# Optimization experiments

Hardware: AMD Instinct MI355X
Metric: run time of the kernel (lower is better)

Reference implementation:

```python
import jax, jax.numpy as jnp
import numpy as np

NEG_BIG = -9e15
ALPHA = 0.2  # LeakyReLU negative slope
B, N, F_IN, F_OUT = 8, 2048, 128, 128


def setup_inputs() -> dict:
    key = jax.random.key(0)
    k1, k2, k3, k4 = jax.random.split(key, 4)
    inp = jax.random.normal(k1, (B, N, F_IN), dtype=jnp.float32)
    adj = jax.random.randint(k2, (B, N, N), 0, 2, dtype=jnp.int32)
    W = 0.02 * jax.random.normal(k3, (F_OUT, F_IN), dtype=jnp.float32)  # nn.Linear weight [out,in]
    a = 0.02 * jax.random.normal(k4, (1, 2 * F_OUT), dtype=jnp.float32)  # attention vector [1, 2F]
    return {"input": inp, "adj": adj, "W": W, "a": a}


def reference(input, adj, W, a):
    # h = input @ W^T : [B, N, F_OUT]
    h = jnp.einsum("bnf,of->bno", input, W)
    f_out = h.shape[-1]
    # Decompose a . [h_i || h_j] = (h_i . a1) + (h_j . a2) -- same math as the
    # explicit repeat_interleave/repeat/cat, without the O(N^2 * 2F) tensor.
    a1 = a[0, :f_out]
    a2 = a[0, f_out:]
    s1 = h @ a1  # [B, N] score for source node i
    s2 = h @ a2  # [B, N] score for target node j
    e = jax.nn.leaky_relu(s1[:, :, None] + s2[:, None, :], negative_slope=ALPHA)  # [B,N,N]
    masked = jnp.where(adj > 0, e, NEG_BIG)
    attention = jax.nn.softmax(masked, axis=-1)
    # dropout p=0.0 (eval) -> identity
    h_prime = jnp.einsum("bnm,bmo->bno", attention, h)
    return h_prime
```

## Files before the change

kernel.cpp:

```cpp
#include <hip/hip_runtime.h>
#include <stdint.h>


#define B_ 8
#define N_ 2048
#define FD 128
#define ALPHA_ 0.2f
#define TJ 64
#define NCHUNK (N_ / TJ)
#define CHUNK_U4 1024

typedef __attribute__((ext_vector_type(8))) short short8;
typedef __attribute__((ext_vector_type(4))) float f32x4;

#define HCHUNK(o, jc) ((((o) * 16) + ((jc) ^ ((o) & 15))) * 8)
#define HC64(o, jc) ((o) * 8 + ((jc) ^ ((o) & 7)))

__device__ __forceinline__ float bf2f(unsigned short u) {
    union { uint32_t i; float f; } v; v.i = ((uint32_t)u) << 16; return v.f;
}
__device__ __forceinline__ unsigned short f2bf(float f) {
    union { float f; uint32_t i; } v; v.f = f;
    uint32_t x = v.i;
    uint32_t r = (x + 0x7fffu + ((x >> 16) & 1u)) >> 16;
    return (unsigned short)r;
}

__global__ __launch_bounds__(256) void gat_h(
    const float* __restrict__ x,
    const float* __restrict__ W,
    const float* __restrict__ a,
    unsigned short* __restrict__ hT,
    float* __restrict__ s1o, float* __restrict__ s2o)
{
    __shared__ __align__(16) unsigned short Wlds[FD * FD];

    const int bid = blockIdx.x;
    const int tid = threadIdx.x;
    const int w = tid >> 6;
    const int lane = tid & 63;
    const int m = lane & 15;
    const int quad = lane >> 4;
    const int arow = bid * 64 + w * 16 + m;

#pragma unroll
    for (int it = 0; it < 8; it++) {
        int cid = it * 256 + tid;
        int o = cid >> 4, kc = cid & 15;
        const float* wp = W + (size_t)o * FD + kc * 8;
        float4 w0 = *(const float4*)wp;
        float4 w1 = *(const float4*)(wp + 4);
        uint4 pk;
        pk.x = (uint32_t)f2bf(w0.x) | ((uint32_t)f2bf(w0.y) << 16);
        pk.y = (uint32_t)f2bf(w0.z) | ((uint32_t)f2bf(w0.w) << 16);
        pk.z = (uint32_t)f2bf(w1.x) | ((uint32_t)f2bf(w1.y) << 16);
        pk.w = (uint32_t)f2bf(w1.z) | ((uint32_t)f2bf(w1.w) << 16);
        *(uint4*)&Wlds[HCHUNK(o, kc)] = pk;
    }
    __syncthreads();

    f32x4 acc[8];
#pragma unroll
    for (int ot = 0; ot < 8; ot++) acc[ot] = (f32x4){0.f, 0.f, 0.f, 0.f};

#pragma unroll
    for (int ks = 0; ks < 4; ks++) {
        const float* xp = x + (size_t)arow * FD + ks * 32 + quad * 8;
        float4 x0 = *(const float4*)xp;
        float4 x1 = *(const float4*)(xp + 4);
        float xv[8] = {x0.x, x0.y, x0.z, x0.w, x1.x, x1.y, x1.z, x1.w};
        union { unsigned short us[8]; short8 v; } ahi, alo;
#pragma unroll
        for (int jj = 0; jj < 8; jj++) {
            unsigned short hi = f2bf(xv[jj]);
            ahi.us[jj] = hi;
            alo.us[jj] = f2bf(xv[jj] - bf2f(hi));
        }
#pragma unroll
        for (int ot = 0; ot < 8; ot++) {
            union { uint4 u; short8 v; } bw;
            bw.u = *(const uint4*)&Wlds[HCHUNK(ot * 16 + m, ks * 4 + quad)];
            acc[ot] = __builtin_amdgcn_mfma_f32_16x16x32_bf16(ahi.v, bw.v, acc[ot], 0, 0, 0);
            acc[ot] = __builtin_amdgcn_mfma_f32_16x16x32_bf16(alo.v, bw.v, acc[ot], 0, 0, 0);
        }
    }

    const int rc0 = bid * 64 + w * 16 + quad * 4;
    const int bb = rc0 >> 11;
    const int jb = rc0 & (N_ - 1);
    const int kc = jb >> 6;
    const int jcl = (jb & 63) >> 3;
    const int off = jb & 7;
    unsigned short* hTb = hT + (size_t)bb * FD * N_ + (size_t)kc * (CHUNK_U4 * 8);
    float s1p[4] = {0.f, 0.f, 0.f, 0.f};
    float s2p[4] = {0.f, 0.f, 0.f, 0.f};
#pragma unroll
    for (int ot = 0; ot < 8; ot++) {
        const int o = ot * 16 + m;
        uint2 pk;
        pk.x = (uint32_t)f2bf(acc[ot][0]) | ((uint32_t)f2bf(acc[ot][1]) << 16);
        pk.y = (uint32_t)f2bf(acc[ot][2]) | ((uint32_t)f2bf(acc[ot][3]) << 16);
        *(uint2*)(hTb + (size_t)HC64(o, jcl) * 8 + off) = pk;
        float a1v = a[o], a2v = a[FD + o];
#pragma unroll
        for (int r = 0; r < 4; r++) {
            s1p[r] += acc[ot][r] * a1v;
            s2p[r] += acc[ot][r] * a2v;
        }
    }
#pragma unroll
    for (int offx = 8; offx >= 1; offx >>= 1) {
#pragma unroll
        for (int r = 0; r < 4; r++) {
            s1p[r] += __shfl_xor(s1p[r], offx);
            s2p[r] += __shfl_xor(s2p[r], offx);
        }
    }
    if (m == 0) {
#pragma unroll
        for (int r = 0; r < 4; r++) {
            s1o[rc0 + r] = s1p[r];
            s2o[rc0 + r] = s2p[r];
        }
    }
}

__global__ __launch_bounds__(128) void gat_attn(
    const int* __restrict__ adj,
    const unsigned short* __restrict__ hT,
    const float* __restrict__ s1,
    const float* __restrict__ s2,
    float* __restrict__ out)
{
    __shared__ __align__(16) uint4 hbuf[2][CHUNK_U4];

    const int bid = blockIdx.x;
    const int b = bid >> 6;
    const int i0 = (bid & 63) * 32;
    const int tid = threadIdx.x;
    const int lane = tid & 63;
    const int w = tid >> 6;
    const int m = lane & 15;
    const int quad = lane >> 4;

    const int irow = i0 + w * 16 + m;
    const float s1v = s1[b * N_ + irow];
    const int* adjrow = adj + ((size_t)(b * N_ + irow)) * N_;
    const uint4* hTc = (const uint4*)(hT + (size_t)b * FD * N_);
    const float* s2b = s2 + b * N_;

    int4 acur[4];
#pragma unroll
    for (int ks = 0; ks < 2; ks++) {
        acur[2 * ks]     = *(const int4*)(adjrow + ks * 32 + quad * 8);
        acur[2 * ks + 1] = *(const int4*)(adjrow + ks * 32 + quad * 8 + 4);
    }
    {
        uint4 g[8];
#pragma unroll
        for (int it = 0; it < 8; it++) g[it] = hTc[it * 128 + tid];
#pragma unroll
        for (int it = 0; it < 8; it++) hbuf[0][it * 128 + tid] = g[it];
    }
    __syncthreads();

    f32x4 acc[8];
#pragma unroll
    for (int ot = 0; ot < 8; ot++) acc[ot] = (f32x4){0.f, 0.f, 0.f, 0.f};
    float rs_loc = 0.f;

    for (int k = 0; k < NCHUNK; k++) {
        const int buf = k & 1;
        const bool more = (k + 1 < NCHUNK);
        int4 anext[4];
        uint4 gn[8];
        if (more) {
            const int j1 = (k + 1) * TJ;
#pragma unroll
            for (int ks = 0; ks < 2; ks++) {
                anext[2 * ks]     = *(const int4*)(adjrow + j1 + ks * 32 + quad * 8);
                anext[2 * ks + 1] = *(const int4*)(adjrow + j1 + ks * 32 + quad * 8 + 4);
            }
#pragma unroll
            for (int it = 0; it < 8; it++)
                gn[it] = hTc[(size_t)(k + 1) * CHUNK_U4 + it * 128 + tid];
        }

#pragma unroll
        for (int ks = 0; ks < 2; ks++) {
            float4 sa = *(const float4*)(s2b + k * TJ + ks * 32 + quad * 8);
            float4 sb = *(const float4*)(s2b + k * TJ + ks * 32 + quad * 8 + 4);
            float sarr[8] = {sa.x, sa.y, sa.z, sa.w, sb.x, sb.y, sb.z, sb.w};
            int4 A0 = acur[2 * ks], A1 = acur[2 * ks + 1];
            int aarr[8] = {A0.x, A0.y, A0.z, A0.w, A1.x, A1.y, A1.z, A1.w};
            union { unsigned short us[8]; short8 v; } af;
#pragma unroll
            for (int jj = 0; jj < 8; jj++) {
                float e = s1v + sarr[jj];
                e = (e > 0.f) ? e : (ALPHA_ * e);
                float p = (aarr[jj] > 0) ? __expf(e) : 0.f;
                rs_loc += p;
                af.us[jj] = f2bf(p);
            }
            const int jc = ks * 4 + quad;
#pragma unroll
            for (int ot = 0; ot < 8; ot++) {
                const int o = ot * 16 + m;
                union { uint4 u; short8 v; } bf;
                bf.u = *(const uint4*)&hbuf[buf][HC64(o, jc)];
                acc[ot] = __builtin_amdgcn_mfma_f32_16x16x32_bf16(af.v, bf.v, acc[ot], 0, 0, 0);
            }
        }

        if (more) {
#pragma unroll
            for (int it = 0; it < 8; it++) hbuf[buf ^ 1][it * 128 + tid] = gn[it];
            __syncthreads();
#pragma unroll
            for (int q = 0; q < 4; q++) acur[q] = anext[q];
        }
    }

    rs_loc += __shfl_xor(rs_loc, 16);
    rs_loc += __shfl_xor(rs_loc, 32);
    float rinv[4];
#pragma unroll
    for (int r = 0; r < 4; r++) rinv[r] = 1.0f / __shfl(rs_loc, quad * 4 + r);

    float* outp = out + (size_t)(b * N_ + i0 + w * 16) * FD;
#pragma unroll
    for (int ot = 0; ot < 8; ot++) {
        const int col = ot * 16 + m;
#pragma unroll
        for (int r = 0; r < 4; r++) {
            outp[(size_t)(quad * 4 + r) * FD + col] = acc[ot][r] * rinv[r];
        }
    }
}

extern "C" void kernel_launch(void* const* d_in, const int* in_sizes, int n_in,
                              void* d_out, int out_size, void* d_ws, size_t ws_size,
                              hipStream_t stream) {
    const void* xv = d_in[0];
    const void* adjv = d_in[1];
    const void* Wv = d_in[2];
    const void* av = d_in[3];
    for (int i = 0; i < n_in; i++) {
        switch (in_sizes[i]) {
            case 2097152:  xv = d_in[i]; break;
            case 33554432: adjv = d_in[i]; break;
            case 16384:    Wv = d_in[i]; break;
            case 256:      av = d_in[i]; break;
            default: break;
        }
    }
    const float* x = (const float*)xv;
    const int* adj = (const int*)adjv;
    const float* W = (const float*)Wv;
    const float* a = (const float*)av;
    float* out = (float*)d_out;

    char* p = (char*)d_ws;
    unsigned short* hT = (unsigned short*)p;  p += (size_t)B_ * FD * N_ * 2;
    float* s1 = (float*)p;                    p += (size_t)B_ * N_ * 4;
    float* s2 = (float*)p;

    gat_h<<<256, 256, 0, stream>>>(x, W, a, hT, s1, s2);
    gat_attn<<<512, 128, 0, stream>>>(adj, hT, s1, s2, out);
}
```

Baseline: 252.1 us.

## Split attention key range across warp pairs and load h directly to LDS

The attention kernel now uses 256 threads per block. Two wave pairs each process half of the key (j) range, and their partial accumulators and row sums are merged through shared memory at the end. The h tiles are staged with global_load_lds, which copies straight from global memory into LDS without passing through registers, and s2 values are prefetched into registers one chunk ahead. This aims to raise parallelism and memory-level overlap on the adjacency stream, at the cost of doubled LDS use, an extra barrier every iteration, and a final reduction step.

```diff
diff --git a/kernel.cpp b/kernel.cpp
--- a/kernel.cpp
+++ b/kernel.cpp
@@ -7,7 +7,7 @@
 #define FD 128
 #define ALPHA_ 0.2f
 #define TJ 64
-#define NCHUNK (N_ / TJ)
+#define NCHL 16
 #define CHUNK_U4 1024
 
 typedef __attribute__((ext_vector_type(8))) short short8;
@@ -24,6 +24,12 @@
     uint32_t x = v.i;
     uint32_t r = (x + 0x7fffu + ((x >> 16) & 1u)) >> 16;
     return (unsigned short)r;
+}
+
+__device__ __forceinline__ void gl2lds16(const uint4* g, uint4* l) {
+    __builtin_amdgcn_global_load_lds(
+        (const __attribute__((address_space(1))) uint32_t*)g,
+        (__attribute__((address_space(3))) uint32_t*)l, 16, 0, 0);
 }
 
 __global__ __launch_bounds__(256) void gat_h(
@@ -125,14 +131,14 @@
     }
 }
 
-__global__ __launch_bounds__(128) void gat_attn(
+__global__ __launch_bounds__(256, 2) void gat_attn(
     const int* __restrict__ adj,
     const unsigned short* __restrict__ hT,
     const float* __restrict__ s1,
     const float* __restrict__ s2,
     float* __restrict__ out)
 {
-    __shared__ __align__(16) uint4 hbuf[2][CHUNK_U4];
+    __shared__ __align__(16) uint4 hbuf[2][2][CHUNK_U4];
 
     const int bid = blockIdx.x;
     const int b = bid >> 6;
@@ -140,27 +146,29 @@
     const int tid = threadIdx.x;
     const int lane = tid & 63;
     const int w = tid >> 6;
+    const int jh = w >> 1;
+    const int rh = w & 1;
     const int m = lane & 15;
     const int quad = lane >> 4;
 
-    const int irow = i0 + w * 16 + m;
+    const int irow = i0 + rh * 16 + m;
     const float s1v = s1[b * N_ + irow];
-    const int* adjrow = adj + ((size_t)(b * N_ + irow)) * N_;
-    const uint4* hTc = (const uint4*)(hT + (size_t)b * FD * N_);
-    const float* s2b = s2 + b * N_;
-
+    const int* adjrow = adj + ((size_t)(b * N_ + irow)) * N_ + jh * 1024;
+    const uint4* hTc = (const uint4*)(hT + (size_t)b * FD * N_)
+                       + (size_t)jh * NCHL * CHUNK_U4;
+    const float* s2b = s2 + b * N_ + jh * 1024;
+
+#pragma unroll
+    for (int it = 0; it < 8; it++)
+        gl2lds16(&hTc[it * 128 + rh * 64 + lane], &hbuf[jh][0][it * 128 + rh * 64]);
     int4 acur[4];
+    float4 scur[4];
 #pragma unroll
     for (int ks = 0; ks < 2; ks++) {
         acur[2 * ks]     = *(const int4*)(adjrow + ks * 32 + quad * 8);
         acur[2 * ks + 1] = *(const int4*)(adjrow + ks * 32 + quad * 8 + 4);
-    }
-    {
-        uint4 g[8];
-#pragma unroll
-        for (int it = 0; it < 8; it++) g[it] = hTc[it * 128 + tid];
-#pragma unroll
-        for (int it = 0; it < 8; it++) hbuf[0][it * 128 + tid] = g[it];
+        scur[2 * ks]     = *(const float4*)(s2b + ks * 32 + quad * 8);
+        scur[2 * ks + 1] = *(const float4*)(s2b + ks * 32 + quad * 8 + 4);
     }
     __syncthreads();
 
@@ -169,27 +177,29 @@
     for (int ot = 0; ot < 8; ot++) acc[ot] = (f32x4){0.f, 0.f, 0.f, 0.f};
     float rs_loc = 0.f;
 
-    for (int k = 0; k < NCHUNK; k++) {
+    for (int k = 0; k < NCHL; k++) {
         const int buf = k & 1;
-        const bool more = (k + 1 < NCHUNK);
+        const bool more = (k + 1 < NCHL);
         int4 anext[4];
-        uint4 gn[8];
+        float4 snext[4];
         if (more) {
+#pragma unroll
+            for (int it = 0; it < 8; it++)
+                gl2lds16(&hTc[(size_t)(k + 1) * CHUNK_U4 + it * 128 + rh * 64 + lane],
+                         &hbuf[jh][buf ^ 1][it * 128 + rh * 64]);
             const int j1 = (k + 1) * TJ;
 #pragma unroll
             for (int ks = 0; ks < 2; ks++) {
                 anext[2 * ks]     = *(const int4*)(adjrow + j1 + ks * 32 + quad * 8);
                 anext[2 * ks + 1] = *(const int4*)(adjrow + j1 + ks * 32 + quad * 8 + 4);
-            }
-#pragma unroll
-            for (int it = 0; it < 8; it++)
-                gn[it] = hTc[(size_t)(k + 1) * CHUNK_U4 + it * 128 + tid];
+                snext[2 * ks]     = *(const float4*)(s2b + j1 + ks * 32 + quad * 8);
+                snext[2 * ks + 1] = *(const float4*)(s2b + j1 + ks * 32 + quad * 8 + 4);
+            }
         }
 
 #pragma unroll
         for (int ks = 0; ks < 2; ks++) {
-            float4 sa = *(const float4*)(s2b + k * TJ + ks * 32 + quad * 8);
-            float4 sb = *(const float4*)(s2b + k * TJ + ks * 32 + quad * 8 + 4);
+            float4 sa = scur[2 * ks], sb = scur[2 * ks + 1];
             float sarr[8] = {sa.x, sa.y, sa.z, sa.w, sb.x, sb.y, sb.z, sb.w};
             int4 A0 = acur[2 * ks], A1 = acur[2 * ks + 1];
             int aarr[8] = {A0.x, A0.y, A0.z, A0.w, A1.x, A1.y, A1.z, A1.w};
@@ -207,33 +217,46 @@
             for (int ot = 0; ot < 8; ot++) {
                 const int o = ot * 16 + m;
                 union { uint4 u; short8 v; } bf;
-                bf.u = *(const uint4*)&hbuf[buf][HC64(o, jc)];
+                bf.u = *(const uint4*)&hbuf[jh][buf][HC64(o, jc)];
                 acc[ot] = __builtin_amdgcn_mfma_f32_16x16x32_bf16(af.v, bf.v, acc[ot], 0, 0, 0);
             }
         }
 
+        __syncthreads();
         if (more) {
 #pragma unroll
-            for (int it = 0; it < 8; it++) hbuf[buf ^ 1][it * 128 + tid] = gn[it];
-            __syncthreads();
-#pragma unroll
-            for (int q = 0; q < 4; q++) acur[q] = anext[q];
-        }
-    }
-
+            for (int q = 0; q < 4; q++) { acur[q] = anext[q]; scur[q] = snext[q]; }
+        }
+    }
+
+    float* xch = (float*)&hbuf[0][0][0];
     rs_loc += __shfl_xor(rs_loc, 16);
     rs_loc += __shfl_xor(rs_loc, 32);
-    float rinv[4];
-#pragma unroll
-    for (int r = 0; r < 4; r++) rinv[r] = 1.0f / __shfl(rs_loc, quad * 4 + r);
-
-    float* outp = out + (size_t)(b * N_ + i0 + w * 16) * FD;
-#pragma unroll
-    for (int ot = 0; ot < 8; ot++) {
-        const int col = ot * 16 + m;
-#pragma unroll
-        for (int r = 0; r < 4; r++) {
-            outp[(size_t)(quad * 4 + r) * FD + col] = acc[ot][r] * rinv[r];
+    if (jh == 1) {
+#pragma unroll
+        for (int ot = 0; ot < 8; ot++)
+#pragma unroll
+            for (int r = 0; r < 4; r++)
+                xch[rh * 2048 + (quad * 4 + r) * 128 + ot * 16 + m] = acc[ot][r];
+        if (quad == 0) xch[4096 + rh * 16 + m] = rs_loc;
+    }
+    __syncthreads();
+    if (jh == 0) {
+        float rinv[4];
+#pragma unroll
+        for (int r = 0; r < 4; r++) {
+            const int p = quad * 4 + r;
+            rinv[r] = 1.0f / (__shfl(rs_loc, p) + xch[4096 + rh * 16 + p]);
+        }
+        float* outp = out + (size_t)(b * N_ + i0 + rh * 16) * FD;
+#pragma unroll
+        for (int ot = 0; ot < 8; ot++) {
+            const int col = ot * 16 + m;
+#pragma unroll
+            for (int r = 0; r < 4; r++) {
+                float v = acc[ot][r] + xch[rh * 2048 + (quad * 4 + r) * 128 + col];
+                outp[(size_t)(quad * 4 + r) * FD + col] = v * rinv[r];
+            }
         }
     }
 }
@@ -266,5 +289,5 @@
     float* s2 = (float*)p;
 
     gat_h<<<256, 256, 0, stream>>>(x, W, a, hT, s1, s2);
-    gat_attn<<<512, 128, 0, stream>>>(adj, hT, s1, s2, out);
-}
+    gat_attn<<<512, 256, 0, stream>>>(adj, hT, s1, s2, out);
+}
```

Result: faster. 217.0 us (-13.9%).
